# Optimization experiments

Measured on AMD Instinct MI355X. Metric: run time of the kernel, lower is better.

Reference implementation:

```python
import jax, jax.numpy as jnp
import numpy as np

D_MODEL = 1024
NUM_HEADS = 16
D_K = D_MODEL // NUM_HEADS
MAX_SEQ_LEN = 2048
THETA = 10000.0


def rotation_matrix_table(theta, d_k, max_seq_len):
    # [max_seq_len, d_k, d_k] block-diagonal 2x2 rotation matrices,
    # same math as the torch reference's generate_rotation_matrix.
    pos = jnp.arange(max_seq_len, dtype=jnp.float32)            # [S]
    kidx = jnp.arange(d_k // 2, dtype=jnp.float32)              # [d_k/2]
    angles = pos[:, None] / (theta ** (2.0 * kidx / d_k))       # [S, d_k/2]
    cos, sin = jnp.cos(angles), jnp.sin(angles)
    rot = jnp.zeros((max_seq_len, d_k, d_k), dtype=jnp.float32)
    ev = jnp.arange(0, d_k, 2)
    od = ev + 1
    rot = rot.at[:, ev, ev].set(cos)
    rot = rot.at[:, ev, od].set(-sin)
    rot = rot.at[:, od, ev].set(sin)
    rot = rot.at[:, od, od].set(cos)
    return rot


def setup_inputs() -> dict:
    key = jax.random.key(0)
    k0, k1, k2, k3, k4 = jax.random.split(key, 5)
    B, S = 4, 2048
    std = np.sqrt(2.0 / (D_MODEL + D_MODEL))
    return {
        "in_features": jax.random.normal(k0, (B, S, D_MODEL), dtype=jnp.float32),
        "wq": jax.random.normal(k1, (D_MODEL, D_MODEL), dtype=jnp.float32) * std,
        "wk": jax.random.normal(k2, (D_MODEL, D_MODEL), dtype=jnp.float32) * std,
        "wv": jax.random.normal(k3, (D_MODEL, D_MODEL), dtype=jnp.float32) * std,
        "wo": jax.random.normal(k4, (D_MODEL, D_MODEL), dtype=jnp.float32) * std,
    }


def reference(in_features, wq, wk, wv, wo):
    B, S, _ = in_features.shape
    H, Dk = NUM_HEADS, D_K
    # QKV projections (weights stored [out, in], applied as x @ W.T)
    q = in_features @ wq.T
    k = in_features @ wk.T
    v = in_features @ wv.T
    # [B, H, S, Dk]
    q = q.reshape(B, S, H, Dk).transpose(0, 2, 1, 3)
    k = k.reshape(B, S, H, Dk).transpose(0, 2, 1, 3)
    v = v.reshape(B, S, H, Dk).transpose(0, 2, 1, 3)
    # RoPE via dense per-position rotation matrix (faithful to source)
    rot = rotation_matrix_table(THETA, Dk, MAX_SEQ_LEN)[:S]     # [S, Dk, Dk]
    q = jnp.einsum("sde,bhse->bhsd", rot, q)
    k = jnp.einsum("sde,bhse->bhsd", rot, k)
    # scaled dot-product attention with causal mask
    scores = jnp.einsum("bhqd,bhkd->bhqk", q, k) / np.sqrt(Dk)
    causal = jnp.tril(jnp.ones((S, S), dtype=bool))             # True = keep
    scores = jnp.where(causal[None, None], scores, -jnp.inf)
    attn = jax.nn.softmax(scores, axis=-1)
    out = jnp.einsum("bhqk,bhkd->bhqd", attn, v)
    out = out.transpose(0, 2, 1, 3).reshape(B, S, H * Dk)
    return out @ wo.T
```

## Files before the change

### kernel.cpp

```cpp
#include <hip/hip_runtime.h>

#define SEQ     2048
#define DMODEL  1024
#define NHEADS  16
#define DKH     64
#define BATCH   4

typedef __bf16 bf16x8 __attribute__((ext_vector_type(8)));
typedef float  f32x4  __attribute__((ext_vector_type(4)));
typedef float  f32x16 __attribute__((ext_vector_type(16)));

static __device__ __forceinline__ unsigned short f2bf(float x) {
  unsigned int u = __float_as_uint(x);
  u += 0x7fffu + ((u >> 16) & 1u);
  return (unsigned short)(u >> 16);
}
static __device__ __forceinline__ float bf2f(unsigned short b) {
  return __uint_as_float(((unsigned int)b) << 16);
}
static __device__ __forceinline__ void gload_lds16(const void* g, void* lds) {
  __builtin_amdgcn_global_load_lds((const __attribute__((address_space(1))) void*)g,
                                   (__attribute__((address_space(3))) void*)lds,
                                   16, 0, 0);
}
static __device__ __forceinline__ f32x4 mfma16(bf16x8 a, bf16x8 b, f32x4 c) {
  return __builtin_amdgcn_mfma_f32_16x16x32_bf16(a, b, c, 0, 0, 0);
}
static __device__ __forceinline__ f32x16 mfma32(bf16x8 a, bf16x8 b, f32x16 c) {
  return __builtin_amdgcn_mfma_f32_32x32x16_bf16(a, b, c, 0, 0, 0);
}
static __device__ __forceinline__ unsigned cvtpk_bf16(float lo, float hi) {
  unsigned r;
  asm("v_cvt_pk_bf16_f32 %0, %1, %2" : "=v"(r) : "v"(lo), "v"(hi));
  return r;
}

__global__ void cast_kernel(const float* __restrict__ src,
                            unsigned short* __restrict__ dst, int n4) {
  int i = blockIdx.x * 256 + threadIdx.x;
  if (i >= n4) return;
  float4 v = ((const float4*)src)[i];
  ushort4 o;
  o.x = f2bf(v.x); o.y = f2bf(v.y); o.z = f2bf(v.z); o.w = f2bf(v.w);
  ((ushort4*)dst)[i] = o;
}

__global__ void cast4_kernel(const float* __restrict__ s0, const float* __restrict__ s1,
                             const float* __restrict__ s2, const float* __restrict__ s3,
                             unsigned short* __restrict__ d0, unsigned short* __restrict__ d1,
                             unsigned short* __restrict__ d2, unsigned short* __restrict__ d3,
                             int n4) {
  int i = blockIdx.x * 256 + threadIdx.x;
  if (i >= n4) return;
  const float* s = (blockIdx.y == 0) ? s0 : (blockIdx.y == 1) ? s1 : (blockIdx.y == 2) ? s2 : s3;
  unsigned short* d = (blockIdx.y == 0) ? d0 : (blockIdx.y == 1) ? d1 : (blockIdx.y == 2) ? d2 : d3;
  float4 v = ((const float4*)s)[i];
  ushort4 o;
  o.x = f2bf(v.x); o.y = f2bf(v.y); o.z = f2bf(v.z); o.w = f2bf(v.w);
  ((ushort4*)d)[i] = o;
}

template<int EPI>
__global__ __launch_bounds__(256)
void gemm_bt(const unsigned short* __restrict__ A,
             const unsigned short* __restrict__ W0,
             const unsigned short* __restrict__ W1,
             const unsigned short* __restrict__ W2,
             unsigned short* __restrict__ O0,
             unsigned short* __restrict__ O1,
             unsigned short* __restrict__ O2,
             float* __restrict__ Of)
{
  __shared__ unsigned short smem[4][128*64];
  const int tid = threadIdx.x;
  const int lane = tid & 63, w = tid >> 6;
  const int wm = w >> 1, wn = w & 1;
  const int l31 = lane & 31, lg2 = lane >> 5;

  const int NWG = (EPI == 0) ? 1536 : 512;
  const int CPX = NWG / 8;
  const int lgid = (blockIdx.x & 7) * CPX + (blockIdx.x >> 3);
  const int n0 = (lgid & 7) * 128;
  const int m0 = ((lgid >> 3) & 63) * 128;
  const int z  = (EPI == 0) ? (lgid >> 9) : 0;
  const unsigned short* Bw = (EPI == 0)
      ? ((z == 0) ? W0 : ((z == 1) ? W1 : W2)) : W0;

  f32x16 acc[2][2];
  #pragma unroll
  for (int a = 0; a < 2; ++a)
    #pragma unroll
    for (int b = 0; b < 2; ++b)
      #pragma unroll
      for (int r = 0; r < 16; ++r)
        acc[a][b][r] = 0.f;

  auto STAGE = [&](int buf, int t) {
    const int k0 = t * 64;
    #pragma unroll
    for (int it = 0; it < 4; ++it) {
      int c = it*4 + w;
      int off16 = c*64 + lane;
      int r = off16 >> 3, p = off16 & 7;
      int s = p ^ (r & 7) ^ ((r >> 3) & 3);
      gload_lds16(A  + (size_t)(m0 + r)*DMODEL + k0 + s*8, (char*)smem[buf]     + c*1024);
      gload_lds16(Bw + (size_t)(n0 + r)*DMODEL + k0 + s*8, (char*)smem[2 + buf] + c*1024);
    }
  };

  const int NT = DMODEL / 64;
  STAGE(0, 0);
  STAGE(1, 1);

  for (int t = 0; t < NT; ++t) {
    const int cur = t & 1;
    if (t == NT - 1) asm volatile("s_waitcnt vmcnt(0)" ::: "memory");
    else             asm volatile("s_waitcnt vmcnt(8)" ::: "memory");
    __builtin_amdgcn_s_barrier();
    __builtin_amdgcn_sched_barrier(0);

    #pragma unroll
    for (int ks = 0; ks < 4; ++ks) {
      bf16x8 af[2], bg[2];
      #pragma unroll
      for (int bi = 0; bi < 2; ++bi) {
        int row = wm*64 + bi*32 + l31;
        int sp = (ks*2 + lg2) ^ (row & 7) ^ ((row >> 3) & 3);
        af[bi] = *(const bf16x8*)((const char*)smem[cur] + row*128 + sp*16);
      }
      #pragma unroll
      for (int bj = 0; bj < 2; ++bj) {
        int row = wn*64 + bj*32 + l31;
        int sp = (ks*2 + lg2) ^ (row & 7) ^ ((row >> 3) & 3);
        bg[bj] = *(const bf16x8*)((const char*)smem[2 + cur] + row*128 + sp*16);
      }
      __builtin_amdgcn_s_setprio(1);
      #pragma unroll
      for (int bi = 0; bi < 2; ++bi)
        #pragma unroll
        for (int bj = 0; bj < 2; ++bj)
          acc[bi][bj] = mfma32(af[bi], bg[bj], acc[bi][bj]);
      __builtin_amdgcn_s_setprio(0);
    }

    __builtin_amdgcn_sched_barrier(0);
    __builtin_amdgcn_s_barrier();
    __builtin_amdgcn_sched_barrier(0);
    if (t + 2 < NT) STAGE(cur, t + 2);
  }

  if (EPI == 1) {
    #pragma unroll
    for (int bi = 0; bi < 2; ++bi)
      #pragma unroll
      for (int bj = 0; bj < 2; ++bj)
        #pragma unroll
        for (int r = 0; r < 16; ++r) {
          int m = m0 + wm*64 + bi*32 + (r & 3) + 8*(r >> 2) + 4*lg2;
          int n = n0 + wn*64 + bj*32 + l31;
          Of[(size_t)m*DMODEL + n] = acc[bi][bj][r];
        }
    return;
  }

  unsigned short* Odst = (z == 0) ? O0 : ((z == 1) ? O1 : O2);

  if (z == 2) {
    unsigned short* tb = (unsigned short*)smem;
    #pragma unroll
    for (int bi = 0; bi < 2; ++bi)
      #pragma unroll
      for (int bj = 0; bj < 2; ++bj) {
        int n_loc = wn*64 + bj*32 + l31;
        #pragma unroll
        for (int g = 0; g < 4; ++g) {
          int m_loc = wm*64 + bi*32 + 8*g + 4*lg2;
          ushort4 pk;
          pk.x = f2bf(acc[bi][bj][g*4 + 0]);
          pk.y = f2bf(acc[bi][bj][g*4 + 1]);
          pk.z = f2bf(acc[bi][bj][g*4 + 2]);
          pk.w = f2bf(acc[bi][bj][g*4 + 3]);
          *(ushort4*)(tb + n_loc*136 + m_loc) = pk;
        }
      }
    __syncthreads();
    const int bb  = m0 >> 11;
    const int sq0 = m0 & (SEQ - 1);
    const size_t obase = (size_t)bb * NHEADS * DKH * SEQ;
    #pragma unroll
    for (int it = 0; it < 8; ++it) {
      int nn = it*16 + (tid >> 4);
      int cc = tid & 15;
      bf16x8 v8 = *(const bf16x8*)(tb + nn*136 + cc*8);
      int hh = (n0 + nn) >> 6;
      int dk = nn & 63;
      *(bf16x8*)&Odst[obase + ((size_t)hh*DKH + dk)*SEQ + sq0 + cc*8] = v8;
    }
  } else {
    float invf2[2];
    #pragma unroll
    for (int bj = 0; bj < 2; ++bj)
      invf2[bj] = exp2f(-0.41524101186092029f * (float)((bj*32 + l31) >> 1));
    #pragma unroll
    for (int bi = 0; bi < 2; ++bi)
      #pragma unroll
      for (int bj = 0; bj < 2; ++bj)
        #pragma unroll
        for (int r = 0; r < 16; ++r) {
          int m = m0 + wm*64 + bi*32 + (r & 3) + 8*(r >> 2) + 4*lg2;
          int n = n0 + wn*64 + bj*32 + l31;
          float v = acc[bi][bj][r];
          int b = m >> 11, sq = m & (SEQ-1), hh = n >> 6, dk = n & 63;
          float prt = __shfl_xor(v, 1);
          float ang = (float)sq * invf2[bj];
          float sn, cs;
          __sincosf(ang, &sn, &cs);
          float out = (l31 & 1) ? (sn*prt + cs*v) : (cs*v - sn*prt);
          if (z == 0) out *= 0.18033688011112043f;
          Odst[(((size_t)b*NHEADS + hh)*SEQ + sq)*DKH + dk] = f2bf(out);
        }
  }
}

__global__ __launch_bounds__(512)
void attn_kernel(const unsigned short* __restrict__ Qg,
                 const unsigned short* __restrict__ Kg,
                 const unsigned short* __restrict__ Vtg,
                 unsigned short* __restrict__ Og)
{
  const int lgid = (blockIdx.x & 7) * 64 + (blockIdx.x >> 3);
  const int px = lgid & 7;
  const int bh = lgid >> 3;
  const int tid = threadIdx.x;
  const int lane = tid & 63, w = tid >> 6;
  const int li = lane & 15, lg = lane >> 4;
  const float THRL2 = 11.0f;

  __shared__ unsigned short sK[2][64*64];
  __shared__ unsigned short sV[2][64*64];
  __shared__ unsigned short sP[8][16*72];
  unsigned short* sPw = sP[w];

  const size_t bhBase = (size_t)bh * SEQ * DKH;
  const f32x4 fz = {0.f, 0.f, 0.f, 0.f};

  auto STAGE = [&](int buf, int t) {
    const int kv0 = t * 64;
    int off16 = w*64 + lane;
    int r = off16 >> 3, p = off16 & 7;
    int s = p ^ (r & 7);
    gload_lds16(Kg  + bhBase + (size_t)(kv0 + r)*DKH + s*8, (char*)sK[buf] + w*1024);
    gload_lds16(Vtg + bhBase + (size_t)r*SEQ + kv0 + s*8,   (char*)sV[buf] + w*1024);
  };

  #pragma unroll 1
  for (int pass = 0; pass < 2; ++pass) {
    const int qt = pass ? (15 - px) : px;
    const int q0 = qt * 128;
    const int myrow0 = q0 + w*16;
    const int qrow = myrow0 + li;

    bf16x8 qf[2];
    {
      const unsigned short* qp = Qg + bhBase + (size_t)qrow*DKH + lg*8;
      qf[0] = *(const bf16x8*)qp;
      qf[1] = *(const bf16x8*)(qp + 32);
    }

    f32x4 acc_o[4];
    #pragma unroll
    for (int nt = 0; nt < 4; ++nt) acc_o[nt] = fz;
    float m_r = -1e30f;
    float ls  = 0.f;

    const int nt_stage = 2*qt + 2;
    const int last_t  = 2*qt + (w >= 4 ? 1 : 0);

    STAGE(0, 0);
    STAGE(1, 1);

    for (int t = 0; t < nt_stage; ++t) {
      const int cur = t & 1;
      if (t == nt_stage - 1) asm volatile("s_waitcnt vmcnt(0)" ::: "memory");
      else                   asm volatile("s_waitcnt vmcnt(2)" ::: "memory");
      __builtin_amdgcn_s_barrier();
      __builtin_amdgcn_sched_barrier(0);

      if (t <= last_t) {
        const int kv0 = t * 64;
        f32x4 sc[4];
        #pragma unroll
        for (int nt = 0; nt < 4; ++nt) sc[nt] = fz;
        __builtin_amdgcn_s_setprio(1);
        #pragma unroll
        for (int kf = 0; kf < 2; ++kf) {
          #pragma unroll
          for (int nt = 0; nt < 4; ++nt) {
            int row = nt*16 + li;
            int sp = (kf*4 + lg) ^ (row & 7);
            bf16x8 kb = *(const bf16x8*)(sK[cur] + row*64 + sp*8);
            sc[nt] = mfma16(kb, qf[kf], sc[nt]);
          }
        }
        __builtin_amdgcn_s_setprio(0);

        if (t == last_t) {
          #pragma unroll
          for (int nt = 0; nt < 4; ++nt)
            #pragma unroll
            for (int kr = 0; kr < 4; ++kr) {
              int kv = kv0 + nt*16 + lg*4 + kr;
              if (kv > qrow) sc[nt][kr] = -1e30f;
            }
        }

        float pm = sc[0][0];
        #pragma unroll
        for (int nt = 0; nt < 4; ++nt)
          #pragma unroll
          for (int kr = 0; kr < 4; ++kr)
            pm = fmaxf(pm, sc[nt][kr]);
        if (__any(pm > m_r + THRL2)) {
          float m2 = pm;
          m2 = fmaxf(m2, __shfl_xor(m2, 16));
          m2 = fmaxf(m2, __shfl_xor(m2, 32));
          float mn = fmaxf(m_r, m2);
          float scl = __builtin_amdgcn_exp2f(m_r - mn);
          m_r = mn;
          ls *= scl;
          float sclk[4];
          #pragma unroll
          for (int kr = 0; kr < 4; ++kr)
            sclk[kr] = __shfl(scl, lg*4 + kr);
          #pragma unroll
          for (int nt = 0; nt < 4; ++nt)
            #pragma unroll
            for (int kr = 0; kr < 4; ++kr)
              acc_o[nt][kr] *= sclk[kr];
        }

        float rs = 0.f;
        #pragma unroll
        for (int nt = 0; nt < 4; ++nt)
          #pragma unroll
          for (int kr = 0; kr < 4; ++kr) {
            float pv = __builtin_amdgcn_exp2f(sc[nt][kr] - m_r);
            sc[nt][kr] = pv;
            rs += pv;
          }
        rs += __shfl_xor(rs, 16);
        rs += __shfl_xor(rs, 32);
        ls += rs;

        #pragma unroll
        for (int nt = 0; nt < 4; ++nt) {
          uint2 pk;
          pk.x = cvtpk_bf16(sc[nt][0], sc[nt][1]);
          pk.y = cvtpk_bf16(sc[nt][2], sc[nt][3]);
          *(uint2*)(sPw + li*72 + nt*16 + lg*4) = pk;
        }

        bf16x8 pa0 = *(const bf16x8*)(sPw + li*72 + 0*32 + lg*8);
        bf16x8 pa1 = *(const bf16x8*)(sPw + li*72 + 1*32 + lg*8);

        __builtin_amdgcn_s_setprio(1);
        #pragma unroll
        for (int nt = 0; nt < 4; ++nt) {
          int rr = nt*16 + li;
          int sp0 = (0*4 + lg) ^ (rr & 7);
          bf16x8 vb0 = *(const bf16x8*)(sV[cur] + rr*64 + sp0*8);
          acc_o[nt] = mfma16(pa0, vb0, acc_o[nt]);
        }
        #pragma unroll
        for (int nt = 0; nt < 4; ++nt) {
          int rr = nt*16 + li;
          int sp1 = (1*4 + lg) ^ (rr & 7);
          bf16x8 vb1 = *(const bf16x8*)(sV[cur] + rr*64 + sp1*8);
          acc_o[nt] = mfma16(pa1, vb1, acc_o[nt]);
        }
        __builtin_amdgcn_s_setprio(0);
      }

      __builtin_amdgcn_sched_barrier(0);
      __builtin_amdgcn_s_barrier();
      __builtin_amdgcn_sched_barrier(0);
      if (t + 2 < nt_stage) STAGE(cur, t + 2);
    }

    const int b = bh >> 4, hh = bh & 15;
    #pragma unroll
    for (int kr = 0; kr < 4; ++kr) {
      float lsr = __shfl(ls, lg*4 + kr);
      float inv = __builtin_amdgcn_rcpf(lsr);
      int srow = myrow0 + lg*4 + kr;
      size_t orow = ((size_t)b*SEQ + srow)*DMODEL + (size_t)hh*DKH;
      #pragma unroll
      for (int nt = 0; nt < 4; ++nt)
        Og[orow + nt*16 + li] = f2bf(acc_o[nt][kr] * inv);
    }
  }
}

extern "C" void kernel_launch(void* const* d_in, const int* in_sizes, int n_in,
                              void* d_out, int out_size, void* d_ws, size_t ws_size,
                              hipStream_t stream)
{
  (void)in_sizes; (void)n_in; (void)out_size; (void)ws_size;
  const float* X  = (const float*)d_in[0];
  const float* Wq = (const float*)d_in[1];
  const float* Wk = (const float*)d_in[2];
  const float* Wv = (const float*)d_in[3];
  const float* Wo = (const float*)d_in[4];

  char* ws = (char*)d_ws;
  const size_t SZ_X = (size_t)8192 * 1024 * 2;
  const size_t SZ_W = (size_t)1024 * 1024 * 2;
  unsigned short* Xb  = (unsigned short*)(ws);
  unsigned short* Wqb = (unsigned short*)(ws + SZ_X);
  unsigned short* Wkb = (unsigned short*)(ws + SZ_X + 1*SZ_W);
  unsigned short* Wvb = (unsigned short*)(ws + SZ_X + 2*SZ_W);
  unsigned short* Wob = (unsigned short*)(ws + SZ_X + 3*SZ_W);
  unsigned short* Vtb = (unsigned short*)(ws + SZ_X + 4*SZ_W);
  unsigned short* Qb  = (unsigned short*)d_out;
  unsigned short* Kb  = Qb + (size_t)8192 * 1024;
  unsigned short* Ob  = Xb;

  cast_kernel<<<8192, 256, 0, stream>>>(X, Xb, 8388608/4);
  cast4_kernel<<<dim3(1024, 4), 256, 0, stream>>>(Wq, Wk, Wv, Wo,
                                                  Wqb, Wkb, Wvb, Wob, 1048576/4);

  gemm_bt<0><<<1536, 256, 0, stream>>>(Xb, Wqb, Wkb, Wvb, Qb, Kb, Vtb, nullptr);
  attn_kernel<<<512, 512, 0, stream>>>(Qb, Kb, Vtb, Ob);
  gemm_bt<1><<<512, 256, 0, stream>>>(Ob, Wob, nullptr, nullptr,
                                      nullptr, nullptr, nullptr,
                                      (float*)d_out);
}
```

Before: 166.3 us.

## Process two adjacent query tiles per block sharing each staged K/V tile

Each attention block used to run two passes over complementary query tiles (px and 15-px), streaming K/V separately for each. It now handles two adjacent query tiles (2i and 2i+1) in a single KV sweep, so every staged K/V tile in LDS is reused by both tiles' compute. This removes one pass's worth of K/V global loads and pipeline prologue. The cost is that work per block is no longer balanced, since blocks with large i do far more work than blocks with small i. Ordering heavy blocks first (i = 7 - ...) is meant to soften the tail, and keeping two accumulator sets raises register pressure.

```diff
diff --git a/kernel.cpp b/kernel.cpp
--- a/kernel.cpp
+++ b/kernel.cpp
@@ -229,7 +229,7 @@
                  unsigned short* __restrict__ Og)
 {
   const int lgid = (blockIdx.x & 7) * 64 + (blockIdx.x >> 3);
-  const int px = lgid & 7;
+  const int i  = 7 - (lgid & 7);
   const int bh = lgid >> 3;
   const int tid = threadIdx.x;
   const int lane = tid & 63, w = tid >> 6;
@@ -253,151 +253,164 @@
     gload_lds16(Vtg + bhBase + (size_t)r*SEQ + kv0 + s*8,   (char*)sV[buf] + w*1024);
   };
 
+  const int rowA0 = (2*i)*128 + w*16;
+  const int rowB0 = (2*i + 1)*128 + w*16;
+  const int qrowA = rowA0 + li;
+  const int qrowB = rowB0 + li;
+
+  bf16x8 qfA[2], qfB[2];
+  {
+    const unsigned short* qpA = Qg + bhBase + (size_t)qrowA*DKH + lg*8;
+    qfA[0] = *(const bf16x8*)qpA;
+    qfA[1] = *(const bf16x8*)(qpA + 32);
+    const unsigned short* qpB = Qg + bhBase + (size_t)qrowB*DKH + lg*8;
+    qfB[0] = *(const bf16x8*)qpB;
+    qfB[1] = *(const bf16x8*)(qpB + 32);
+  }
+
+  f32x4 accA[4], accB[4];
+  #pragma unroll
+  for (int nt = 0; nt < 4; ++nt) { accA[nt] = fz; accB[nt] = fz; }
+  float mA = -1e30f, mB = -1e30f;
+  float lsA = 0.f, lsB = 0.f;
+
+  const int nt_stage = 4*i + 4;
+  const int lastA = 4*i + (w >= 4 ? 1 : 0);
+  const int lastB = 4*i + 2 + (w >= 4 ? 1 : 0);
+
+  auto COMPUTE = [&](int cur, int kv0, const bf16x8* qf, f32x4* acc_o,
+                     float& m_r, float& ls, int qrow, bool domask) {
+    f32x4 sc[4];
+    #pragma unroll
+    for (int nt = 0; nt < 4; ++nt) sc[nt] = fz;
+    __builtin_amdgcn_s_setprio(1);
+    #pragma unroll
+    for (int kf = 0; kf < 2; ++kf) {
+      #pragma unroll
+      for (int nt = 0; nt < 4; ++nt) {
+        int row = nt*16 + li;
+        int sp = (kf*4 + lg) ^ (row & 7);
+        bf16x8 kb = *(const bf16x8*)(sK[cur] + row*64 + sp*8);
+        sc[nt] = mfma16(kb, qf[kf], sc[nt]);
+      }
+    }
+    __builtin_amdgcn_s_setprio(0);
+
+    if (domask) {
+      #pragma unroll
+      for (int nt = 0; nt < 4; ++nt)
+        #pragma unroll
+        for (int kr = 0; kr < 4; ++kr) {
+          int kv = kv0 + nt*16 + lg*4 + kr;
+          if (kv > qrow) sc[nt][kr] = -1e30f;
+        }
+    }
+
+    float pm = sc[0][0];
+    #pragma unroll
+    for (int nt = 0; nt < 4; ++nt)
+      #pragma unroll
+      for (int kr = 0; kr < 4; ++kr)
+        pm = fmaxf(pm, sc[nt][kr]);
+    if (__any(pm > m_r + THRL2)) {
+      float m2 = pm;
+      m2 = fmaxf(m2, __shfl_xor(m2, 16));
+      m2 = fmaxf(m2, __shfl_xor(m2, 32));
+      float mn = fmaxf(m_r, m2);
+      float scl = __builtin_amdgcn_exp2f(m_r - mn);
+      m_r = mn;
+      ls *= scl;
+      float sclk[4];
+      #pragma unroll
+      for (int kr = 0; kr < 4; ++kr)
+        sclk[kr] = __shfl(scl, lg*4 + kr);
+      #pragma unroll
+      for (int nt = 0; nt < 4; ++nt)
+        #pragma unroll
+        for (int kr = 0; kr < 4; ++kr)
+          acc_o[nt][kr] *= sclk[kr];
+    }
+
+    float rs = 0.f;
+    #pragma unroll
+    for (int nt = 0; nt < 4; ++nt)
+      #pragma unroll
+      for (int kr = 0; kr < 4; ++kr) {
+        float pv = __builtin_amdgcn_exp2f(sc[nt][kr] - m_r);
+        sc[nt][kr] = pv;
+        rs += pv;
+      }
+    rs += __shfl_xor(rs, 16);
+    rs += __shfl_xor(rs, 32);
+    ls += rs;
+
+    #pragma unroll
+    for (int nt = 0; nt < 4; ++nt) {
+      uint2 pk;
+      pk.x = cvtpk_bf16(sc[nt][0], sc[nt][1]);
+      pk.y = cvtpk_bf16(sc[nt][2], sc[nt][3]);
+      *(uint2*)(sPw + li*72 + nt*16 + lg*4) = pk;
+    }
+    bf16x8 pa0 = *(const bf16x8*)(sPw + li*72 + 0*32 + lg*8);
+    bf16x8 pa1 = *(const bf16x8*)(sPw + li*72 + 1*32 + lg*8);
+
+    __builtin_amdgcn_s_setprio(1);
+    #pragma unroll
+    for (int nt = 0; nt < 4; ++nt) {
+      int rr = nt*16 + li;
+      int sp0 = (0*4 + lg) ^ (rr & 7);
+      bf16x8 vb0 = *(const bf16x8*)(sV[cur] + rr*64 + sp0*8);
+      acc_o[nt] = mfma16(pa0, vb0, acc_o[nt]);
+    }
+    #pragma unroll
+    for (int nt = 0; nt < 4; ++nt) {
+      int rr = nt*16 + li;
+      int sp1 = (1*4 + lg) ^ (rr & 7);
+      bf16x8 vb1 = *(const bf16x8*)(sV[cur] + rr*64 + sp1*8);
+      acc_o[nt] = mfma16(pa1, vb1, acc_o[nt]);
+    }
+    __builtin_amdgcn_s_setprio(0);
+  };
+
+  STAGE(0, 0);
+  STAGE(1, 1);
+
   #pragma unroll 1
-  for (int pass = 0; pass < 2; ++pass) {
-    const int qt = pass ? (15 - px) : px;
-    const int q0 = qt * 128;
-    const int myrow0 = q0 + w*16;
-    const int qrow = myrow0 + li;
-
-    bf16x8 qf[2];
-    {
-      const unsigned short* qp = Qg + bhBase + (size_t)qrow*DKH + lg*8;
-      qf[0] = *(const bf16x8*)qp;
-      qf[1] = *(const bf16x8*)(qp + 32);
-    }
-
-    f32x4 acc_o[4];
-    #pragma unroll
-    for (int nt = 0; nt < 4; ++nt) acc_o[nt] = fz;
-    float m_r = -1e30f;
-    float ls  = 0.f;
-
-    const int nt_stage = 2*qt + 2;
-    const int last_t  = 2*qt + (w >= 4 ? 1 : 0);
-
-    STAGE(0, 0);
-    STAGE(1, 1);
-
-    for (int t = 0; t < nt_stage; ++t) {
-      const int cur = t & 1;
-      if (t == nt_stage - 1) asm volatile("s_waitcnt vmcnt(0)" ::: "memory");
-      else                   asm volatile("s_waitcnt vmcnt(2)" ::: "memory");
-      __builtin_amdgcn_s_barrier();
-      __builtin_amdgcn_sched_barrier(0);
-
-      if (t <= last_t) {
-        const int kv0 = t * 64;
-        f32x4 sc[4];
-        #pragma unroll
-        for (int nt = 0; nt < 4; ++nt) sc[nt] = fz;
-        __builtin_amdgcn_s_setprio(1);
-        #pragma unroll
-        for (int kf = 0; kf < 2; ++kf) {
-          #pragma unroll
-          for (int nt = 0; nt < 4; ++nt) {
-            int row = nt*16 + li;
-            int sp = (kf*4 + lg) ^ (row & 7);
-            bf16x8 kb = *(const bf16x8*)(sK[cur] + row*64 + sp*8);
-            sc[nt] = mfma16(kb, qf[kf], sc[nt]);
-          }
-        }
-        __builtin_amdgcn_s_setprio(0);
-
-        if (t == last_t) {
-          #pragma unroll
-          for (int nt = 0; nt < 4; ++nt)
-            #pragma unroll
-            for (int kr = 0; kr < 4; ++kr) {
-              int kv = kv0 + nt*16 + lg*4 + kr;
-              if (kv > qrow) sc[nt][kr] = -1e30f;
-            }
-        }
-
-        float pm = sc[0][0];
-        #pragma unroll
-        for (int nt = 0; nt < 4; ++nt)
-          #pragma unroll
-          for (int kr = 0; kr < 4; ++kr)
-            pm = fmaxf(pm, sc[nt][kr]);
-        if (__any(pm > m_r + THRL2)) {
-          float m2 = pm;
-          m2 = fmaxf(m2, __shfl_xor(m2, 16));
-          m2 = fmaxf(m2, __shfl_xor(m2, 32));
-          float mn = fmaxf(m_r, m2);
-          float scl = __builtin_amdgcn_exp2f(m_r - mn);
-          m_r = mn;
-          ls *= scl;
-          float sclk[4];
-          #pragma unroll
-          for (int kr = 0; kr < 4; ++kr)
-            sclk[kr] = __shfl(scl, lg*4 + kr);
-          #pragma unroll
-          for (int nt = 0; nt < 4; ++nt)
-            #pragma unroll
-            for (int kr = 0; kr < 4; ++kr)
-              acc_o[nt][kr] *= sclk[kr];
-        }
-
-        float rs = 0.f;
-        #pragma unroll
-        for (int nt = 0; nt < 4; ++nt)
-          #pragma unroll
-          for (int kr = 0; kr < 4; ++kr) {
-            float pv = __builtin_amdgcn_exp2f(sc[nt][kr] - m_r);
-            sc[nt][kr] = pv;
-            rs += pv;
-          }
-        rs += __shfl_xor(rs, 16);
-        rs += __shfl_xor(rs, 32);
-        ls += rs;
-
-        #pragma unroll
-        for (int nt = 0; nt < 4; ++nt) {
-          uint2 pk;
-          pk.x = cvtpk_bf16(sc[nt][0], sc[nt][1]);
-          pk.y = cvtpk_bf16(sc[nt][2], sc[nt][3]);
-          *(uint2*)(sPw + li*72 + nt*16 + lg*4) = pk;
-        }
-
-        bf16x8 pa0 = *(const bf16x8*)(sPw + li*72 + 0*32 + lg*8);
-        bf16x8 pa1 = *(const bf16x8*)(sPw + li*72 + 1*32 + lg*8);
-
-        __builtin_amdgcn_s_setprio(1);
-        #pragma unroll
-        for (int nt = 0; nt < 4; ++nt) {
-          int rr = nt*16 + li;
-          int sp0 = (0*4 + lg) ^ (rr & 7);
-          bf16x8 vb0 = *(const bf16x8*)(sV[cur] + rr*64 + sp0*8);
-          acc_o[nt] = mfma16(pa0, vb0, acc_o[nt]);
-        }
-        #pragma unroll
-        for (int nt = 0; nt < 4; ++nt) {
-          int rr = nt*16 + li;
-          int sp1 = (1*4 + lg) ^ (rr & 7);
-          bf16x8 vb1 = *(const bf16x8*)(sV[cur] + rr*64 + sp1*8);
-          acc_o[nt] = mfma16(pa1, vb1, acc_o[nt]);
-        }
-        __builtin_amdgcn_s_setprio(0);
-      }
-
-      __builtin_amdgcn_sched_barrier(0);
-      __builtin_amdgcn_s_barrier();
-      __builtin_amdgcn_sched_barrier(0);
-      if (t + 2 < nt_stage) STAGE(cur, t + 2);
-    }
-
-    const int b = bh >> 4, hh = bh & 15;
-    #pragma unroll
-    for (int kr = 0; kr < 4; ++kr) {
-      float lsr = __shfl(ls, lg*4 + kr);
-      float inv = __builtin_amdgcn_rcpf(lsr);
-      int srow = myrow0 + lg*4 + kr;
-      size_t orow = ((size_t)b*SEQ + srow)*DMODEL + (size_t)hh*DKH;
-      #pragma unroll
-      for (int nt = 0; nt < 4; ++nt)
-        Og[orow + nt*16 + li] = f2bf(acc_o[nt][kr] * inv);
-    }
+  for (int t = 0; t < nt_stage; ++t) {
+    const int cur = t & 1;
+    if (t == nt_stage - 1) asm volatile("s_waitcnt vmcnt(0)" ::: "memory");
+    else                   asm volatile("s_waitcnt vmcnt(2)" ::: "memory");
+    __builtin_amdgcn_s_barrier();
+    __builtin_amdgcn_sched_barrier(0);
+
+    const int kv0 = t * 64;
+    if (t <= lastB) COMPUTE(cur, kv0, qfB, accB, mB, lsB, qrowB, t == lastB);
+    if (t <= lastA) COMPUTE(cur, kv0, qfA, accA, mA, lsA, qrowA, t == lastA);
+
+    __builtin_amdgcn_sched_barrier(0);
+    __builtin_amdgcn_s_barrier();
+    __builtin_amdgcn_sched_barrier(0);
+    if (t + 2 < nt_stage) STAGE(cur, t + 2);
+  }
+
+  const int b = bh >> 4, hh = bh & 15;
+  #pragma unroll
+  for (int kr = 0; kr < 4; ++kr) {
+    float lsrA = __shfl(lsA, lg*4 + kr);
+    float invA = __builtin_amdgcn_rcpf(lsrA);
+    int srowA = rowA0 + lg*4 + kr;
+    size_t orowA = ((size_t)b*SEQ + srowA)*DMODEL + (size_t)hh*DKH;
+    #pragma unroll
+    for (int nt = 0; nt < 4; ++nt)
+      Og[orowA + nt*16 + li] = f2bf(accA[nt][kr] * invA);
+
+    float lsrB = __shfl(lsB, lg*4 + kr);
+    float invB = __builtin_amdgcn_rcpf(lsrB);
+    int srowB = rowB0 + lg*4 + kr;
+    size_t orowB = ((size_t)b*SEQ + srowB)*DMODEL + (size_t)hh*DKH;
+    #pragma unroll
+    for (int nt = 0; nt < 4; ++nt)
+      Og[orowB + nt*16 + li] = f2bf(accB[nt][kr] * invB);
   }
 }
 
```

Result: slower. 195.1 us (+17.3%).
